# Optimization experiments

Measured on AMD Instinct MI355X. Metric: run time of the kernel, lower is better.

## Reference

```python
import jax, jax.numpy as jnp
import numpy as np

ROW = COL = 8   # unfold tile size
KS = 5          # gaussian raster kernel size
C1 = 6          # high-freq feature split

def conv2d(x, w, b=None, pad=0):
    y = jax.lax.conv_general_dilated(x, w, (1, 1), [(pad, pad), (pad, pad)],
                                     dimension_numbers=('NCHW', 'OIHW', 'NCHW'))
    if b is not None:
        y = y + b[None, :, None, None]
    return y

def unfold_tiles(x, r, c):
    # non-overlapping Unfold(kernel=(r,c), stride=(r,c)) -> [B*L, C, r, c]
    B, C, H, W = x.shape
    x = x.reshape(B, C, H // r, r, W // c, c).transpose(0, 2, 4, 1, 3, 5)
    return x.reshape(B * (H // r) * (W // c), C, r, c)

def fold_tiles(t, B, C, H, W, r, c):
    t = t.reshape(B, H // r, W // c, C, r, c).transpose(0, 3, 1, 4, 2, 5)
    return t.reshape(B, C, H, W)

def setup_inputs() -> dict:
    key = jax.random.key(0)
    ks = jax.random.split(key, 16)
    B, NF, H, W, P = 32, 48, 128, 128, 81
    inp = {
        'ms': jax.random.normal(ks[0], (B, 4, 32, 32), jnp.float32),
        'feat': jax.random.normal(ks[1], (B, NF, H, W), jnp.float32),
        'V': jax.random.normal(ks[2], (B, NF, H, W), jnp.float32),
        'logits_raw': jax.random.normal(ks[3], (B, P, H, W), jnp.float32),
        'sigma_x': jax.random.uniform(ks[4], (P,), jnp.float32, 0.2, 3.0),
        'sigma_y': jax.random.uniform(ks[5], (P,), jnp.float32, 0.2, 3.0),
        'opacity': jax.random.uniform(ks[6], (P,), jnp.float32, 0.1, 1.0),
        'rho': jax.random.uniform(ks[7], (P,), jnp.float32, -0.9, 0.9),
        'w_v2': jax.random.normal(ks[8], (42, 42, 1, 1), jnp.float32) * 0.05,
        'w_fine': jax.random.normal(ks[9], (4, NF, 3, 3), jnp.float32) * 0.05,
        'b_fine': jax.random.normal(ks[10], (4,), jnp.float32) * 0.05,
        'w_res': jax.random.normal(ks[11], (4, NF, 1, 1), jnp.float32) * 0.05,
        'b_res': jax.random.normal(ks[12], (4,), jnp.float32) * 0.05,
    }
    return inp

def reference(ms, feat, V, logits_raw, sigma_x, sigma_y, opacity, rho,
              w_v2, w_fine, b_fine, w_res, b_res):
    B, nf, H, W = feat.shape
    # soft class assignment (gumbel_softmax tau=1, zero-noise deterministic surrogate)
    logits = jax.nn.softmax(logits_raw, axis=1)
    feat1, lr_feat = feat[:, :C1], feat[:, C1:]
    V1, V2 = V[:, :C1], V[:, C1:]
    # H,W are already multiples of ROW/COL -> bicubic-to-same-size is identity
    uf = unfold_tiles(feat1, ROW, COL)        # [B*L, c1, 8, 8]
    ul = unfold_tiles(logits, ROW, COL)       # [B*L, P, 8, 8]
    uv1 = unfold_tiles(V1, ROW, COL)          # [B*L, c1, 8, 8]
    # weighted gaussian params per in-tile position, averaged over all tiles
    pm = ul.reshape(ul.shape[0], ul.shape[1], -1).mean(axis=0)   # [P, 64]
    wsx = sigma_x @ pm; wsy = sigma_y @ pm                       # [64]
    wop = opacity @ pm; wr = rho @ pm                            # [64]
    # 2x2 covariance per point, analytic inverse
    a = wsx ** 2; bcv = wr * wsx * wsy; d = wsy ** 2
    det = a * d - bcv ** 2
    i00 = d / det; i01 = -bcv / det; i11 = a / det
    ax = jnp.linspace(-5.0, 5.0, KS)
    xx = ax[:, None]; yy = ax[None, :]
    z = -0.5 * (i00[:, None, None] * xx ** 2 + 2.0 * i01[:, None, None] * xx * yy
                + i11[:, None, None] * yy ** 2)
    kern = jnp.exp(z) / (2.0 * jnp.pi * jnp.sqrt(det))[:, None, None]   # [64, KS, KS]
    kern = kern / kern.max(axis=(-2, -1), keepdims=True)
    kern = kern * wop[:, None, None]
    # splat: place each point's kernel centered at its grid position in the 8x8 tile
    pad = KS // 2
    ii = jnp.arange(ROW * COL) // COL
    jj = jnp.arange(ROW * COL) % COL
    canvas = jnp.zeros((ROW + 2 * pad, COL + 2 * pad), kern.dtype)
    place = jax.vmap(lambda k, i, j: jax.lax.dynamic_update_slice(canvas, k, (i, j)))
    K = place(kern, ii, jj)[:, pad:pad + ROW, pad:pad + COL]             # [64, 8, 8]
    colors = uf.reshape(uf.shape[0], C1, ROW * COL)                      # [N, c1, 64]
    rendered = jnp.einsum('ncp,phw->nchw', colors, K) * uv1              # modulate by V1
    hr = fold_tiles(rendered, B, C1, H, W, ROW, COL)                     # [B, c1, H, W]
    # squeeze-style channel attention on low branch, modulated by V2
    gap = lr_feat.mean(axis=(2, 3), keepdims=True)
    attn = jax.nn.sigmoid(conv2d(gap, w_v2))
    lr_mod = lr_feat * attn * V2
    out_feat = jnp.concatenate([hr, lr_mod], axis=1)                     # [B, n_feats, H, W]
    up_ms = jax.image.resize(ms, (B, ms.shape[1], H, W), method='bilinear')
    out = conv2d(out_feat, w_fine, b_fine, pad=1) + conv2d(feat, w_res, b_res) + up_ms
    return out
```

## Files before the change

### kernel.cpp

```cpp
#include <hip/hip_runtime.h>

#define NBATCH 32
#define NFEAT 48
#define C1c 6
#define LRC 42
#define HH 128
#define WW 128
#define HWSZ 16384
#define NP 81
#define NQ 64

#define OFF_PM   0
#define OFF_GAP  5184
#define OFF_K    6528
#define OFF_ATTN 10624
#define OFF_WB   11968
#define OFF_HR   14272

__global__ __launch_bounds__(256) void k_sm1(const float* __restrict__ logits,
                                             float* __restrict__ invbuf) {
    int idx = blockIdx.x * 256 + threadIdx.x;
    int b   = idx >> 14;
    int pos = idx & 16383;
    const float* base = logits + (((size_t)b * NP) << 14) + pos;
    float s = 0.f;
    for (int p = 0; p < NP; ++p)
        s += __expf(base[(size_t)p << 14]);
    invbuf[idx] = 1.f / s;
}

__global__ __launch_bounds__(256) void k_base(const float* __restrict__ feat,
                                              const float* __restrict__ ms,
                                              const float* __restrict__ w_res,
                                              const float* __restrict__ b_fine,
                                              const float* __restrict__ b_res,
                                              float* __restrict__ gap,
                                              float* __restrict__ out) {
    int gid = blockIdx.x;
    int tid = threadIdx.x;
    int b = gid >> 4, strip = gid & 15;
    int row = (strip << 3) + (tid >> 5);
    int x0  = (tid & 31) << 2;
    int poff = (row << 7) + x0;
    int lane = tid & 63;
    const float* fb = feat + (((size_t)b * NFEAT) << 14);
    float a[4][4];
#pragma unroll
    for (int j = 0; j < 4; ++j)
#pragma unroll
        for (int o = 0; o < 4; ++o) a[j][o] = 0.f;
    for (int c = 0; c < NFEAT; ++c) {
        float4 f = *(const float4*)&fb[((size_t)c << 14) + poff];
        float wr0 = w_res[c], wr1 = w_res[NFEAT + c];
        float wr2 = w_res[2 * NFEAT + c], wr3 = w_res[3 * NFEAT + c];
        a[0][0] += wr0 * f.x; a[0][1] += wr1 * f.x; a[0][2] += wr2 * f.x; a[0][3] += wr3 * f.x;
        a[1][0] += wr0 * f.y; a[1][1] += wr1 * f.y; a[1][2] += wr2 * f.y; a[1][3] += wr3 * f.y;
        a[2][0] += wr0 * f.z; a[2][1] += wr1 * f.z; a[2][2] += wr2 * f.z; a[2][3] += wr3 * f.z;
        a[3][0] += wr0 * f.w; a[3][1] += wr1 * f.w; a[3][2] += wr2 * f.w; a[3][3] += wr3 * f.w;
        if (c >= C1c) {
            float s = (f.x + f.y) + (f.z + f.w);
            s += __shfl_xor(s, 1);  s += __shfl_xor(s, 2);  s += __shfl_xor(s, 4);
            s += __shfl_xor(s, 8);  s += __shfl_xor(s, 16); s += __shfl_xor(s, 32);
            if (lane == 0) atomicAdd(&gap[b * LRC + (c - C1c)], s);
        }
    }
    float syf = (row + 0.5f) * 0.25f - 0.5f;
    int y0i = (int)floorf(syf); float fy = syf - (float)y0i;
    int y0c = min(31, max(0, y0i)), y1c = min(31, max(0, y0i + 1));
    float fxv[4]; int x0v[4], x1v[4];
#pragma unroll
    for (int j = 0; j < 4; ++j) {
        float sxf = (x0 + j + 0.5f) * 0.25f - 0.5f;
        int x0i = (int)floorf(sxf);
        fxv[j] = sxf - (float)x0i;
        x0v[j] = min(31, max(0, x0i));
        x1v[j] = min(31, max(0, x0i + 1));
    }
#pragma unroll
    for (int o = 0; o < 4; ++o) {
        const float* mb = ms + ((size_t)(b * 4 + o) << 10);
        float addc = b_fine[o] + b_res[o];
        float res[4];
#pragma unroll
        for (int j = 0; j < 4; ++j) {
            float m00 = mb[(y0c << 5) + x0v[j]], m01 = mb[(y0c << 5) + x1v[j]];
            float m10 = mb[(y1c << 5) + x0v[j]], m11 = mb[(y1c << 5) + x1v[j]];
            float up = (m00 * (1.f - fxv[j]) + m01 * fxv[j]) * (1.f - fy)
                     + (m10 * (1.f - fxv[j]) + m11 * fxv[j]) * fy;
            res[j] = a[j][o] + addc + up;
        }
        *(float4*)&out[(((size_t)(b * 4 + o)) << 14) + poff] =
            make_float4(res[0], res[1], res[2], res[3]);
    }
}

__global__ __launch_bounds__(256) void k_sm2(const float* __restrict__ logits,
                                             const float* __restrict__ invbuf,
                                             float* __restrict__ pm_sum) {
    int bid = blockIdx.x;
    int b = bid / NP, p = bid - b * NP;
    const float* base = logits + ((size_t)(b * NP + p) << 14);
    const float* ib   = invbuf + ((size_t)b << 14);
    int tid = threadIdx.x;
    int r0 = tid >> 5, xt = tid & 31;
    float a0 = 0.f, a1 = 0.f, a2 = 0.f, a3 = 0.f;
    int off = (r0 << 7) + (xt << 2);
#pragma unroll 4
    for (int k = 0; k < 16; ++k) {
        int o2 = off + k * 1024;
        float4 l4 = *(const float4*)&base[o2];
        float4 i4 = *(const float4*)&ib[o2];
        a0 += __expf(l4.x) * i4.x;
        a1 += __expf(l4.y) * i4.y;
        a2 += __expf(l4.z) * i4.z;
        a3 += __expf(l4.w) * i4.w;
    }
#pragma unroll
    for (int m = 2; m <= 16; m <<= 1) {
        a0 += __shfl_xor(a0, m); a1 += __shfl_xor(a1, m);
        a2 += __shfl_xor(a2, m); a3 += __shfl_xor(a3, m);
    }
    if (xt < 2) {
        int qb = p * NQ + (r0 << 3) + ((xt & 1) << 2);
        atomicAdd(&pm_sum[qb + 0], a0);
        atomicAdd(&pm_sum[qb + 1], a1);
        atomicAdd(&pm_sum[qb + 2], a2);
        atomicAdd(&pm_sum[qb + 3], a3);
    }
}

__global__ __launch_bounds__(256) void k_small(const float* __restrict__ pm_sum,
                                               const float* __restrict__ gap_sum,
                                               const float* __restrict__ sigx,
                                               const float* __restrict__ sigy,
                                               const float* __restrict__ opac,
                                               const float* __restrict__ rho,
                                               const float* __restrict__ w_v2,
                                               const float* __restrict__ w_fine,
                                               const float* __restrict__ w_res,
                                               float* __restrict__ Kmat,
                                               float* __restrict__ attn,
                                               float* __restrict__ wbuf) {
    int tid = threadIdx.x;
    if (tid < 64) {
        int q = tid;
        float wsx = 0.f, wsy = 0.f, wop = 0.f, wr = 0.f;
        for (int p = 0; p < NP; ++p) {
            float pv = pm_sum[p * NQ + q] * (1.f / 8192.f);
            wsx += sigx[p] * pv;
            wsy += sigy[p] * pv;
            wop += opac[p] * pv;
            wr  += rho[p]  * pv;
        }
        float a = wsx * wsx, d = wsy * wsy, bc = wr * wsx * wsy;
        float det = a * d - bc * bc;
        float i00 = d / det, i01 = -bc / det, i11 = a / det;
        int iq = q >> 3, jq = q & 7;
        for (int h = 0; h < 8; ++h)
            for (int w = 0; w < 8; ++w) {
                int ki = h - iq + 2, kj = w - jq + 2;
                float val = 0.f;
                if (ki >= 0 && ki < 5 && kj >= 0 && kj < 5) {
                    float xx = -5.f + 2.5f * ki, yy = -5.f + 2.5f * kj;
                    val = wop * __expf(-0.5f * (i00 * xx * xx + 2.f * i01 * xx * yy + i11 * yy * yy));
                }
                Kmat[(q << 6) + (h << 3) + w] = val;
            }
    }
    for (int i = tid; i < NBATCH * LRC; i += 256) {
        int b = i / LRC, co = i % LRC;
        float s = 0.f;
        for (int ci = 0; ci < LRC; ++ci) s += w_v2[co * LRC + ci] * gap_sum[b * LRC + ci];
        s *= (1.f / 16384.f);
        attn[i] = 1.f / (1.f + __expf(-s));
    }
    for (int i = tid; i < NFEAT * 48; i += 256) {
        int c = i / 48, j = i - c * 48;
        float v = 0.f;
        if (j < 36) v = w_fine[(j / 9) * (NFEAT * 9) + c * 9 + (j % 9)];
        else if (j < 40) v = w_res[(j - 36) * NFEAT + c];
        wbuf[i] = v;
    }
}

__global__ __launch_bounds__(256) void k_hr(const float* __restrict__ feat,
                                            const float* __restrict__ V,
                                            const float* __restrict__ Kmat,
                                            float* __restrict__ hrbuf) {
    __shared__ __align__(16) float lK[4096];
    __shared__ __align__(16) float lF[2 * 16 * 128];
    int bid = blockIdx.x;
    int b   = bid / 24;
    int r   = bid - b * 24;
    int strip = r / 3;
    int ch  = (r - strip * 3) * 2;
    int y0  = strip << 4;
    int tid = threadIdx.x;
    {
        const float4* ks = (const float4*)Kmat;
        float4* kd = (float4*)lK;
        for (int i = tid; i < 1024; i += 256) kd[i] = ks[i];
        float4* fd = (float4*)lF;
        const float* fb = feat + (((size_t)b * NFEAT + ch) << 14) + (y0 << 7);
        for (int i = tid; i < 1024; i += 256) {
            int c = i >> 9, rem = i & 511;
            fd[i] = *(const float4*)&fb[((size_t)c << 14) + (rem << 2)];
        }
    }
    __syncthreads();
    int tile = tid >> 3, hrow = tid & 7;
    int tr = tile >> 4, tx = tile & 15;
    float acc[2][8];
#pragma unroll
    for (int c = 0; c < 2; ++c)
#pragma unroll
        for (int j = 0; j < 8; ++j) acc[c][j] = 0.f;
    int fbase = (tr << 3) * 128 + (tx << 3);
    for (int q = 0; q < 64; ++q) {
        int iq = q >> 3, jq = q & 7;
        const float4 k0 = *(const float4*)&lK[(q << 6) + (hrow << 3)];
        const float4 k1 = *(const float4*)&lK[(q << 6) + (hrow << 3) + 4];
#pragma unroll
        for (int c = 0; c < 2; ++c) {
            float col = lF[(c << 11) + fbase + (iq << 7) + jq];
            acc[c][0] += col * k0.x; acc[c][1] += col * k0.y;
            acc[c][2] += col * k0.z; acc[c][3] += col * k0.w;
            acc[c][4] += col * k1.x; acc[c][5] += col * k1.y;
            acc[c][6] += col * k1.z; acc[c][7] += col * k1.w;
        }
    }
    int y = y0 + (tr << 3) + hrow;
#pragma unroll
    for (int c = 0; c < 2; ++c) {
        const float4* vp = (const float4*)(V + (((size_t)b * NFEAT + ch + c) << 14) + ((size_t)y << 7) + (tx << 3));
        float4 v0 = vp[0], v1 = vp[1];
        float4 r0, r1;
        r0.x = acc[c][0] * v0.x; r0.y = acc[c][1] * v0.y; r0.z = acc[c][2] * v0.z; r0.w = acc[c][3] * v0.w;
        r1.x = acc[c][4] * v1.x; r1.y = acc[c][5] * v1.y; r1.z = acc[c][6] * v1.z; r1.w = acc[c][7] * v1.w;
        float4* op = (float4*)(hrbuf + (((size_t)b * C1c + ch + c) << 14) + ((size_t)y << 7) + (tx << 3));
        op[0] = r0; op[1] = r1;
    }
}

#define CHN 6
__global__ __launch_bounds__(512, 4) void k_conv(const float* __restrict__ feat,
                                                 const float* __restrict__ V,
                                                 const float* __restrict__ wbuf,
                                                 const float* __restrict__ hrbuf,
                                                 const float* __restrict__ attn,
                                                 float* __restrict__ out) {
    __shared__ float s_in[2][CHN][18 * 40];
    int bid0 = blockIdx.x;
    int rid  = (bid0 & 7) * 128 + (bid0 >> 3);
    int b    = rid >> 5;
    int t32  = rid & 31;
    int ty0  = (t32 >> 2) << 4;
    int tx0  = (t32 & 3) << 5;
    int tid  = threadIdx.x;
    int grpu = __builtin_amdgcn_readfirstlane(tid >> 8);
    int ct   = tid & 255;
    int rp   = ct >> 5;
    int j    = ct & 31;
    int gx   = tx0 + j;
    int gy0  = ty0 + 2 * rp;
    int cbase = (2 * rp) * 40 + 3 + j;

    int srow = tid >> 5, scol = tid & 31;
    int sg = ((ty0 + srow) << 7) + tx0 + scol;
    int sl = (srow + 1) * 40 + 4 + scol;

    bool hhas = tid < 100;
    int rr, cc;
    if (tid < 34)      { rr = 0;        cc = tid; }
    else if (tid < 68) { rr = 17;       cc = tid - 34; }
    else if (tid < 84) { rr = tid - 67; cc = 0; }
    else               { rr = tid - 83; cc = 33; }
    int hsy = ty0 - 1 + rr, hsx = tx0 - 1 + cc;
    float hfm = (hsy >= 0 && hsy < HH && hsx >= 0 && hsx < WW) ? 1.f : 0.f;
    int hoff = (min(HH - 1, max(0, hsy)) << 7) + min(WW - 1, max(0, hsx));
    int hlds = rr * 40 + 3 + cc;

    const float* atb = attn + b * LRC;
    float a0[4] = {0.f, 0.f, 0.f, 0.f};
    float a1[4] = {0.f, 0.f, 0.f, 0.f};
    float rA[CHN], rB[CHN], rHA[CHN], rHB[CHN], amv[CHN];

#pragma unroll
    for (int k = 0; k < CHN; ++k) {
        const float* hs = hrbuf + (((size_t)(b * C1c + k)) << 14);
        rA[k]  = hs[sg];
        rHA[k] = hhas ? hs[hoff] : 0.f;
    }
#pragma unroll
    for (int k = 0; k < CHN; ++k) {
        s_in[0][k][sl] = rA[k];
        if (hhas) s_in[0][k][hlds] = rHA[k] * hfm;
    }
    int cur = 0;
    for (int t = 0; t < 8; ++t) {
        __syncthreads();
        if (t < 7) {
            int c0 = CHN * (t + 1);
#pragma unroll
            for (int k = 0; k < CHN; ++k) {
                int c = c0 + k;
                const float* fs = feat + (((size_t)(b * NFEAT + c)) << 14);
                const float* vs = V    + (((size_t)(b * NFEAT + c)) << 14);
                rA[k] = fs[sg];
                rB[k] = vs[sg];
                amv[k] = atb[c - C1c];
                rHA[k] = hhas ? fs[hoff] : 0.f;
                rHB[k] = hhas ? vs[hoff] : 0.f;
            }
        }
        int c0c = CHN * t;
        for (int k = 0; k < 3; ++k) {
            int slot = 3 * grpu + k;
            int c = c0c + slot;
            const float* wc = wbuf + c * 48;
            const float* sp = &s_in[cur][slot][cbase];
            float t00 = sp[0],   t01 = sp[1],   t02 = sp[2];
            float t10 = sp[40],  t11 = sp[41],  t12 = sp[42];
            float t20 = sp[80],  t21 = sp[81],  t22 = sp[82];
            float t30 = sp[120], t31 = sp[121], t32 = sp[122];
#pragma unroll
            for (int o = 0; o < 4; ++o) {
                float w0 = wc[o * 9 + 0], w1 = wc[o * 9 + 1], w2 = wc[o * 9 + 2];
                float w3 = wc[o * 9 + 3], w4 = wc[o * 9 + 4], w5 = wc[o * 9 + 5];
                float w6 = wc[o * 9 + 6], w7 = wc[o * 9 + 7], w8 = wc[o * 9 + 8];
                a0[o] += w0 * t00 + w1 * t01 + w2 * t02
                       + w3 * t10 + w4 * t11 + w5 * t12
                       + w6 * t20 + w7 * t21 + w8 * t22;
                a1[o] += w0 * t10 + w1 * t11 + w2 * t12
                       + w3 * t20 + w4 * t21 + w5 * t22
                       + w6 * t30 + w7 * t31 + w8 * t32;
            }
        }
        if (t < 7) {
            int nxt = cur ^ 1;
#pragma unroll
            for (int k = 0; k < CHN; ++k) {
                s_in[nxt][k][sl] = rA[k] * rB[k] * amv[k];
                if (hhas) s_in[nxt][k][hlds] = rHA[k] * rHB[k] * (amv[k] * hfm);
            }
        }
        cur ^= 1;
    }
    __syncthreads();
    float* sm = &s_in[0][0][0];
    int p0 = (2 * rp) * 32 + j, p1 = p0 + 32;
    if (grpu == 1) {
#pragma unroll
        for (int o = 0; o < 4; ++o) { sm[o * 512 + p0] = a0[o]; sm[o * 512 + p1] = a1[o]; }
    }
    __syncthreads();
    if (grpu == 0) {
#pragma unroll
        for (int o = 0; o < 4; ++o) {
            size_t obase = ((size_t)(b * 4 + o)) << 14;
            float* op0 = out + obase + (gy0 << 7) + gx;
            float* op1 = out + obase + ((gy0 + 1) << 7) + gx;
            *op0 = *op0 + a0[o] + sm[o * 512 + p0];
            *op1 = *op1 + a1[o] + sm[o * 512 + p1];
        }
    }
}

extern "C" void kernel_launch(void* const* d_in, const int* in_sizes, int n_in,
                              void* d_out, int out_size, void* d_ws, size_t ws_size,
                              hipStream_t stream) {
    (void)in_sizes; (void)n_in; (void)out_size; (void)ws_size;
    const float* ms     = (const float*)d_in[0];
    const float* feat   = (const float*)d_in[1];
    const float* V      = (const float*)d_in[2];
    const float* logits = (const float*)d_in[3];
    const float* sigx   = (const float*)d_in[4];
    const float* sigy   = (const float*)d_in[5];
    const float* opac   = (const float*)d_in[6];
    const float* rho    = (const float*)d_in[7];
    const float* w_v2   = (const float*)d_in[8];
    const float* w_fine = (const float*)d_in[9];
    const float* b_fine = (const float*)d_in[10];
    const float* w_res  = (const float*)d_in[11];
    const float* b_res  = (const float*)d_in[12];
    float* ws  = (float*)d_ws;
    float* out = (float*)d_out;
    float* inv = ws + OFF_HR;

    hipMemsetAsync(ws + OFF_PM, 0, (size_t)(NP * NQ + NBATCH * LRC) * sizeof(float), stream);
    k_sm1<<<2048, 256, 0, stream>>>(logits, inv);
    k_base<<<512, 256, 0, stream>>>(feat, ms, w_res, b_fine, b_res, ws + OFF_GAP, out);
    k_sm2<<<NBATCH * NP, 256, 0, stream>>>(logits, inv, ws + OFF_PM);
    k_small<<<1, 256, 0, stream>>>(ws + OFF_PM, ws + OFF_GAP, sigx, sigy, opac, rho, w_v2,
                                   w_fine, w_res, ws + OFF_K, ws + OFF_ATTN, ws + OFF_WB);
    k_hr<<<768, 256, 0, stream>>>(feat, V, ws + OFF_K, ws + OFF_HR);
    k_conv<<<1024, 512, 0, stream>>>(feat, V, ws + OFF_WB, ws + OFF_HR, ws + OFF_ATTN, out);
}
```

Baseline: 216.5 us.

## Split softmax denominator into channel-chunked partial sums plus reduction kernel

The per-pixel softmax denominator pass now splits the 81 logit channels into 9 chunks per batch. Each block streams a whole channel plane with float4 loads and writes partial exp-sums to a new workspace region. A second small kernel sums the 9 partials and writes reciprocals. This aims to raise memory-level parallelism and load width over the old one-thread-per-pixel 81-deep strided loop, at the cost of an extra launch and a partial buffer round trip.

Result: slower. 276.2 us (+27.6%).

```diff
diff --git a/kernel.cpp b/kernel.cpp
--- a/kernel.cpp
+++ b/kernel.cpp
@@ -16,17 +16,44 @@
 #define OFF_ATTN 10624
 #define OFF_WB   11968
 #define OFF_HR   14272
+#define OFF_PART (OFF_HR + 4194304)
 
 __global__ __launch_bounds__(256) void k_sm1(const float* __restrict__ logits,
-                                             float* __restrict__ invbuf) {
+                                             float* __restrict__ part) {
+    int bid = blockIdx.x;
+    int b = bid / 9, chunk = bid - b * 9;
+    int p0 = chunk * 9;
+    int tid = threadIdx.x;
+    const float4* lg4 = (const float4*)logits;
+    float4 acc[16];
+#pragma unroll
+    for (int k = 0; k < 16; ++k) acc[k] = make_float4(0.f, 0.f, 0.f, 0.f);
+    for (int i = 0; i < 9; ++i) {
+        const float4* pl = lg4 + ((size_t)(b * NP + p0 + i) << 12);
+#pragma unroll
+        for (int k = 0; k < 16; ++k) {
+            float4 v = pl[(k << 8) + tid];
+            acc[k].x += __expf(v.x); acc[k].y += __expf(v.y);
+            acc[k].z += __expf(v.z); acc[k].w += __expf(v.w);
+        }
+    }
+    float4* pp = (float4*)part + ((size_t)bid << 12);
+#pragma unroll
+    for (int k = 0; k < 16; ++k) pp[(k << 8) + tid] = acc[k];
+}
+
+__global__ __launch_bounds__(256) void k_minv(const float* __restrict__ part,
+                                              float* __restrict__ invbuf) {
     int idx = blockIdx.x * 256 + threadIdx.x;
-    int b   = idx >> 14;
-    int pos = idx & 16383;
-    const float* base = logits + (((size_t)b * NP) << 14) + pos;
-    float s = 0.f;
-    for (int p = 0; p < NP; ++p)
-        s += __expf(base[(size_t)p << 14]);
-    invbuf[idx] = 1.f / s;
+    int b = idx >> 12, i = idx & 4095;
+    const float4* p4 = (const float4*)part;
+    float sx = 0.f, sy = 0.f, sz = 0.f, sw = 0.f;
+#pragma unroll
+    for (int c = 0; c < 9; ++c) {
+        float4 v = p4[((size_t)(b * 9 + c) << 12) + i];
+        sx += v.x; sy += v.y; sz += v.z; sw += v.w;
+    }
+    ((float4*)invbuf)[idx] = make_float4(1.f / sx, 1.f / sy, 1.f / sz, 1.f / sw);
 }
 
 __global__ __launch_bounds__(256) void k_base(const float* __restrict__ feat,
@@ -385,11 +412,13 @@
     const float* b_res  = (const float*)d_in[12];
     float* ws  = (float*)d_ws;
     float* out = (float*)d_out;
-    float* inv = ws + OFF_HR;
+    float* inv  = ws + OFF_HR;
+    float* part = ws + OFF_PART;
 
     hipMemsetAsync(ws + OFF_PM, 0, (size_t)(NP * NQ + NBATCH * LRC) * sizeof(float), stream);
-    k_sm1<<<2048, 256, 0, stream>>>(logits, inv);
+    k_sm1<<<288, 256, 0, stream>>>(logits, part);
     k_base<<<512, 256, 0, stream>>>(feat, ms, w_res, b_fine, b_res, ws + OFF_GAP, out);
+    k_minv<<<512, 256, 0, stream>>>(part, inv);
     k_sm2<<<NBATCH * NP, 256, 0, stream>>>(logits, inv, ws + OFF_PM);
     k_small<<<1, 256, 0, stream>>>(ws + OFF_PM, ws + OFF_GAP, sigx, sigy, opac, rho, w_v2,
                                    w_fine, w_res, ws + OFF_K, ws + OFF_ATTN, ws + OFF_WB);
```

## Split softmax denominator over class chunks and fuse with base conv kernel

Applied to the files above, without the earlier changes.

The softmax sum-of-exp pass is split into three chunks of 27 classes, each computed by separate blocks with hand-written double-buffered dwordx4 loads. These blocks are merged into one launch with the residual conv/upsample blocks so both independent passes run concurrently. A small kernel then sums the three partial results and takes the reciprocal. This adds a partial buffer round trip and an extra launch, in exchange for more parallelism, wider loads and overlap of the two memory-bound passes.

Result: faster. 210.3 us (-2.8%).

```diff
diff --git a/kernel.cpp b/kernel.cpp
--- a/kernel.cpp
+++ b/kernel.cpp
@@ -16,82 +16,121 @@
 #define OFF_ATTN 10624
 #define OFF_WB   11968
 #define OFF_HR   14272
-
-__global__ __launch_bounds__(256) void k_sm1(const float* __restrict__ logits,
-                                             float* __restrict__ invbuf) {
+#define OFF_PART (OFF_HR + 4194304)
+
+typedef float f4 __attribute__((ext_vector_type(4)));
+
+#define GL(dst, ptr) asm volatile("global_load_dwordx4 %0, %1, off" : "=v"(dst) : "v"(ptr))
+#define WAITV2()     asm volatile("s_waitcnt vmcnt(2)" ::: "memory")
+#define WAITV0()     asm volatile("s_waitcnt vmcnt(0)" ::: "memory")
+#define SBAR()       __builtin_amdgcn_sched_barrier(0)
+
+__global__ __launch_bounds__(256) void k_phase1(const float* __restrict__ logits,
+                                                const float* __restrict__ feat,
+                                                const float* __restrict__ ms,
+                                                const float* __restrict__ w_res,
+                                                const float* __restrict__ b_fine,
+                                                const float* __restrict__ b_res,
+                                                float* __restrict__ part,
+                                                float* __restrict__ gap,
+                                                float* __restrict__ out) {
+    int bid = blockIdx.x;
+    int tid = threadIdx.x;
+    if (bid < 768) {
+        int s = bid >> 8;
+        int r = bid & 255;
+        int b = r >> 3, w = r & 7;
+        const float* base = logits + (((size_t)(b * NP + s * 27)) << 14) + (w << 11) + (tid << 3);
+        f4 A0 = {0.f, 0.f, 0.f, 0.f}, A1 = {0.f, 0.f, 0.f, 0.f};
+        f4 c0, c1, n0, n1;
+        GL(c0, base); GL(c1, base + 4);
+        for (int p = 0; p < 26; p += 2) {
+            const float* p1 = base + ((size_t)(p + 1) << 14);
+            GL(n0, p1); GL(n1, p1 + 4);
+            WAITV2(); SBAR();
+            A0.x += __expf(c0.x); A0.y += __expf(c0.y); A0.z += __expf(c0.z); A0.w += __expf(c0.w);
+            A1.x += __expf(c1.x); A1.y += __expf(c1.y); A1.z += __expf(c1.z); A1.w += __expf(c1.w);
+            const float* p2 = base + ((size_t)(p + 2) << 14);
+            GL(c0, p2); GL(c1, p2 + 4);
+            WAITV2(); SBAR();
+            A0.x += __expf(n0.x); A0.y += __expf(n0.y); A0.z += __expf(n0.z); A0.w += __expf(n0.w);
+            A1.x += __expf(n1.x); A1.y += __expf(n1.y); A1.z += __expf(n1.z); A1.w += __expf(n1.w);
+        }
+        WAITV0(); SBAR();
+        A0.x += __expf(c0.x); A0.y += __expf(c0.y); A0.z += __expf(c0.z); A0.w += __expf(c0.w);
+        A1.x += __expf(c1.x); A1.y += __expf(c1.y); A1.z += __expf(c1.z); A1.w += __expf(c1.w);
+        float* pp = part + (size_t)s * 524288 + ((size_t)b << 14) + (w << 11) + (tid << 3);
+        *(f4*)pp = A0;
+        *(f4*)(pp + 4) = A1;
+    } else {
+        int gid = bid - 768;
+        int b = gid >> 4, strip = gid & 15;
+        int row = (strip << 3) + (tid >> 5);
+        int x0  = (tid & 31) << 2;
+        int poff = (row << 7) + x0;
+        int lane = tid & 63;
+        const float* fb = feat + (((size_t)b * NFEAT) << 14);
+        float a[4][4];
+#pragma unroll
+        for (int j = 0; j < 4; ++j)
+#pragma unroll
+            for (int o = 0; o < 4; ++o) a[j][o] = 0.f;
+        for (int c = 0; c < NFEAT; ++c) {
+            float4 f = *(const float4*)&fb[((size_t)c << 14) + poff];
+            float wr0 = w_res[c], wr1 = w_res[NFEAT + c];
+            float wr2 = w_res[2 * NFEAT + c], wr3 = w_res[3 * NFEAT + c];
+            a[0][0] += wr0 * f.x; a[0][1] += wr1 * f.x; a[0][2] += wr2 * f.x; a[0][3] += wr3 * f.x;
+            a[1][0] += wr0 * f.y; a[1][1] += wr1 * f.y; a[1][2] += wr2 * f.y; a[1][3] += wr3 * f.y;
+            a[2][0] += wr0 * f.z; a[2][1] += wr1 * f.z; a[2][2] += wr2 * f.z; a[2][3] += wr3 * f.z;
+            a[3][0] += wr0 * f.w; a[3][1] += wr1 * f.w; a[3][2] += wr2 * f.w; a[3][3] += wr3 * f.w;
+            if (c >= C1c) {
+                float s = (f.x + f.y) + (f.z + f.w);
+                s += __shfl_xor(s, 1);  s += __shfl_xor(s, 2);  s += __shfl_xor(s, 4);
+                s += __shfl_xor(s, 8);  s += __shfl_xor(s, 16); s += __shfl_xor(s, 32);
+                if (lane == 0) atomicAdd(&gap[b * LRC + (c - C1c)], s);
+            }
+        }
+        float syf = (row + 0.5f) * 0.25f - 0.5f;
+        int y0i = (int)floorf(syf); float fy = syf - (float)y0i;
+        int y0c = min(31, max(0, y0i)), y1c = min(31, max(0, y0i + 1));
+        float fxv[4]; int x0v[4], x1v[4];
+#pragma unroll
+        for (int j = 0; j < 4; ++j) {
+            float sxf = (x0 + j + 0.5f) * 0.25f - 0.5f;
+            int x0i = (int)floorf(sxf);
+            fxv[j] = sxf - (float)x0i;
+            x0v[j] = min(31, max(0, x0i));
+            x1v[j] = min(31, max(0, x0i + 1));
+        }
+#pragma unroll
+        for (int o = 0; o < 4; ++o) {
+            const float* mb = ms + ((size_t)(b * 4 + o) << 10);
+            float addc = b_fine[o] + b_res[o];
+            float res[4];
+#pragma unroll
+            for (int j = 0; j < 4; ++j) {
+                float m00 = mb[(y0c << 5) + x0v[j]], m01 = mb[(y0c << 5) + x1v[j]];
+                float m10 = mb[(y1c << 5) + x0v[j]], m11 = mb[(y1c << 5) + x1v[j]];
+                float up = (m00 * (1.f - fxv[j]) + m01 * fxv[j]) * (1.f - fy)
+                         + (m10 * (1.f - fxv[j]) + m11 * fxv[j]) * fy;
+                res[j] = a[j][o] + addc + up;
+            }
+            *(float4*)&out[(((size_t)(b * 4 + o)) << 14) + poff] =
+                make_float4(res[0], res[1], res[2], res[3]);
+        }
+    }
+}
+
+__global__ __launch_bounds__(256) void k_minv(const float* __restrict__ part,
+                                              float* __restrict__ invbuf) {
     int idx = blockIdx.x * 256 + threadIdx.x;
-    int b   = idx >> 14;
-    int pos = idx & 16383;
-    const float* base = logits + (((size_t)b * NP) << 14) + pos;
-    float s = 0.f;
-    for (int p = 0; p < NP; ++p)
-        s += __expf(base[(size_t)p << 14]);
-    invbuf[idx] = 1.f / s;
-}
-
-__global__ __launch_bounds__(256) void k_base(const float* __restrict__ feat,
-                                              const float* __restrict__ ms,
-                                              const float* __restrict__ w_res,
-                                              const float* __restrict__ b_fine,
-                                              const float* __restrict__ b_res,
-                                              float* __restrict__ gap,
-                                              float* __restrict__ out) {
-    int gid = blockIdx.x;
-    int tid = threadIdx.x;
-    int b = gid >> 4, strip = gid & 15;
-    int row = (strip << 3) + (tid >> 5);
-    int x0  = (tid & 31) << 2;
-    int poff = (row << 7) + x0;
-    int lane = tid & 63;
-    const float* fb = feat + (((size_t)b * NFEAT) << 14);
-    float a[4][4];
-#pragma unroll
-    for (int j = 0; j < 4; ++j)
-#pragma unroll
-        for (int o = 0; o < 4; ++o) a[j][o] = 0.f;
-    for (int c = 0; c < NFEAT; ++c) {
-        float4 f = *(const float4*)&fb[((size_t)c << 14) + poff];
-        float wr0 = w_res[c], wr1 = w_res[NFEAT + c];
-        float wr2 = w_res[2 * NFEAT + c], wr3 = w_res[3 * NFEAT + c];
-        a[0][0] += wr0 * f.x; a[0][1] += wr1 * f.x; a[0][2] += wr2 * f.x; a[0][3] += wr3 * f.x;
-        a[1][0] += wr0 * f.y; a[1][1] += wr1 * f.y; a[1][2] += wr2 * f.y; a[1][3] += wr3 * f.y;
-        a[2][0] += wr0 * f.z; a[2][1] += wr1 * f.z; a[2][2] += wr2 * f.z; a[2][3] += wr3 * f.z;
-        a[3][0] += wr0 * f.w; a[3][1] += wr1 * f.w; a[3][2] += wr2 * f.w; a[3][3] += wr3 * f.w;
-        if (c >= C1c) {
-            float s = (f.x + f.y) + (f.z + f.w);
-            s += __shfl_xor(s, 1);  s += __shfl_xor(s, 2);  s += __shfl_xor(s, 4);
-            s += __shfl_xor(s, 8);  s += __shfl_xor(s, 16); s += __shfl_xor(s, 32);
-            if (lane == 0) atomicAdd(&gap[b * LRC + (c - C1c)], s);
-        }
-    }
-    float syf = (row + 0.5f) * 0.25f - 0.5f;
-    int y0i = (int)floorf(syf); float fy = syf - (float)y0i;
-    int y0c = min(31, max(0, y0i)), y1c = min(31, max(0, y0i + 1));
-    float fxv[4]; int x0v[4], x1v[4];
-#pragma unroll
-    for (int j = 0; j < 4; ++j) {
-        float sxf = (x0 + j + 0.5f) * 0.25f - 0.5f;
-        int x0i = (int)floorf(sxf);
-        fxv[j] = sxf - (float)x0i;
-        x0v[j] = min(31, max(0, x0i));
-        x1v[j] = min(31, max(0, x0i + 1));
-    }
-#pragma unroll
-    for (int o = 0; o < 4; ++o) {
-        const float* mb = ms + ((size_t)(b * 4 + o) << 10);
-        float addc = b_fine[o] + b_res[o];
-        float res[4];
-#pragma unroll
-        for (int j = 0; j < 4; ++j) {
-            float m00 = mb[(y0c << 5) + x0v[j]], m01 = mb[(y0c << 5) + x1v[j]];
-            float m10 = mb[(y1c << 5) + x0v[j]], m11 = mb[(y1c << 5) + x1v[j]];
-            float up = (m00 * (1.f - fxv[j]) + m01 * fxv[j]) * (1.f - fy)
-                     + (m10 * (1.f - fxv[j]) + m11 * fxv[j]) * fy;
-            res[j] = a[j][o] + addc + up;
-        }
-        *(float4*)&out[(((size_t)(b * 4 + o)) << 14) + poff] =
-            make_float4(res[0], res[1], res[2], res[3]);
-    }
+    const f4* p4 = (const f4*)part;
+    f4 a = p4[idx];
+    f4 b = p4[idx + 131072];
+    f4 c = p4[idx + 262144];
+    f4 s = a + b + c;
+    f4 r = {1.f / s.x, 1.f / s.y, 1.f / s.z, 1.f / s.w};
+    ((f4*)invbuf)[idx] = r;
 }
 
 __global__ __launch_bounds__(256) void k_sm2(const float* __restrict__ logits,
@@ -385,11 +424,13 @@
     const float* b_res  = (const float*)d_in[12];
     float* ws  = (float*)d_ws;
     float* out = (float*)d_out;
-    float* inv = ws + OFF_HR;
+    float* inv  = ws + OFF_HR;
+    float* part = ws + OFF_PART;
 
     hipMemsetAsync(ws + OFF_PM, 0, (size_t)(NP * NQ + NBATCH * LRC) * sizeof(float), stream);
-    k_sm1<<<2048, 256, 0, stream>>>(logits, inv);
-    k_base<<<512, 256, 0, stream>>>(feat, ms, w_res, b_fine, b_res, ws + OFF_GAP, out);
+    k_phase1<<<768 + 512, 256, 0, stream>>>(logits, feat, ms, w_res, b_fine, b_res,
+                                            part, ws + OFF_GAP, out);
+    k_minv<<<512, 256, 0, stream>>>(part, inv);
     k_sm2<<<NBATCH * NP, 256, 0, stream>>>(logits, inv, ws + OFF_PM);
     k_small<<<1, 256, 0, stream>>>(ws + OFF_PM, ws + OFF_GAP, sigx, sigy, opac, rho, w_v2,
                                    w_fine, w_res, ws + OFF_K, ws + OFF_ATTN, ws + OFF_WB);
```

## Fuse softmax passes into single-read kernel merged with base conv blocks

Applied to the files above, without the earlier changes.

Replaces the two-pass softmax (one kernel for the inverse sums, a second that re-reads logits) with a single pass. Each thread keeps all 81 exponentials in registers, normalises them, and accumulates per-tile sums that are reduced with shuffles and atomics. This kernel is merged with the residual-conv/upsample blocks into one launch, with separate block ranges for each job. It removes a full second read of the logits plus the intermediate inverse buffer. In exchange it uses heavy register arrays (81 accumulators plus 81 exponentials), which can hurt occupancy or spill under launch_bounds(256,2).

Result: faster. 188.7 us, median of 2 (-12.8%).

```diff
diff --git a/kernel.cpp b/kernel.cpp
--- a/kernel.cpp
+++ b/kernel.cpp
@@ -17,115 +17,102 @@
 #define OFF_WB   11968
 #define OFF_HR   14272
 
-__global__ __launch_bounds__(256) void k_sm1(const float* __restrict__ logits,
-                                             float* __restrict__ invbuf) {
-    int idx = blockIdx.x * 256 + threadIdx.x;
-    int b   = idx >> 14;
-    int pos = idx & 16383;
-    const float* base = logits + (((size_t)b * NP) << 14) + pos;
-    float s = 0.f;
-    for (int p = 0; p < NP; ++p)
-        s += __expf(base[(size_t)p << 14]);
-    invbuf[idx] = 1.f / s;
-}
-
-__global__ __launch_bounds__(256) void k_base(const float* __restrict__ feat,
-                                              const float* __restrict__ ms,
-                                              const float* __restrict__ w_res,
-                                              const float* __restrict__ b_fine,
-                                              const float* __restrict__ b_res,
-                                              float* __restrict__ gap,
-                                              float* __restrict__ out) {
-    int gid = blockIdx.x;
+__global__ __launch_bounds__(256, 2) void k_phase1(const float* __restrict__ logits,
+                                                   const float* __restrict__ feat,
+                                                   const float* __restrict__ ms,
+                                                   const float* __restrict__ w_res,
+                                                   const float* __restrict__ b_fine,
+                                                   const float* __restrict__ b_res,
+                                                   float* __restrict__ pm_sum,
+                                                   float* __restrict__ gap,
+                                                   float* __restrict__ out) {
+    int bid = blockIdx.x;
     int tid = threadIdx.x;
-    int b = gid >> 4, strip = gid & 15;
-    int row = (strip << 3) + (tid >> 5);
-    int x0  = (tid & 31) << 2;
-    int poff = (row << 7) + x0;
-    int lane = tid & 63;
-    const float* fb = feat + (((size_t)b * NFEAT) << 14);
-    float a[4][4];
-#pragma unroll
-    for (int j = 0; j < 4; ++j)
-#pragma unroll
-        for (int o = 0; o < 4; ++o) a[j][o] = 0.f;
-    for (int c = 0; c < NFEAT; ++c) {
-        float4 f = *(const float4*)&fb[((size_t)c << 14) + poff];
-        float wr0 = w_res[c], wr1 = w_res[NFEAT + c];
-        float wr2 = w_res[2 * NFEAT + c], wr3 = w_res[3 * NFEAT + c];
-        a[0][0] += wr0 * f.x; a[0][1] += wr1 * f.x; a[0][2] += wr2 * f.x; a[0][3] += wr3 * f.x;
-        a[1][0] += wr0 * f.y; a[1][1] += wr1 * f.y; a[1][2] += wr2 * f.y; a[1][3] += wr3 * f.y;
-        a[2][0] += wr0 * f.z; a[2][1] += wr1 * f.z; a[2][2] += wr2 * f.z; a[2][3] += wr3 * f.z;
-        a[3][0] += wr0 * f.w; a[3][1] += wr1 * f.w; a[3][2] += wr2 * f.w; a[3][3] += wr3 * f.w;
-        if (c >= C1c) {
-            float s = (f.x + f.y) + (f.z + f.w);
-            s += __shfl_xor(s, 1);  s += __shfl_xor(s, 2);  s += __shfl_xor(s, 4);
-            s += __shfl_xor(s, 8);  s += __shfl_xor(s, 16); s += __shfl_xor(s, 32);
-            if (lane == 0) atomicAdd(&gap[b * LRC + (c - C1c)], s);
-        }
-    }
-    float syf = (row + 0.5f) * 0.25f - 0.5f;
-    int y0i = (int)floorf(syf); float fy = syf - (float)y0i;
-    int y0c = min(31, max(0, y0i)), y1c = min(31, max(0, y0i + 1));
-    float fxv[4]; int x0v[4], x1v[4];
-#pragma unroll
-    for (int j = 0; j < 4; ++j) {
-        float sxf = (x0 + j + 0.5f) * 0.25f - 0.5f;
-        int x0i = (int)floorf(sxf);
-        fxv[j] = sxf - (float)x0i;
-        x0v[j] = min(31, max(0, x0i));
-        x1v[j] = min(31, max(0, x0i + 1));
-    }
-#pragma unroll
-    for (int o = 0; o < 4; ++o) {
-        const float* mb = ms + ((size_t)(b * 4 + o) << 10);
-        float addc = b_fine[o] + b_res[o];
-        float res[4];
+    if (bid < 512) {
+        int b   = bid >> 4;
+        int ygp = (bid >> 2) & 3;
+        int qq  = bid & 3;
+        int x   = tid & 127;
+        int yg  = ygp * 2 + (tid >> 7);
+        float acc[NP];
+#pragma unroll
+        for (int p = 0; p < NP; ++p) acc[p] = 0.f;
+        for (int k = 0; k < 4; ++k) {
+            int y = yg + 8 * (qq * 4 + k);
+            const float* base = logits + (size_t)b * NP * HWSZ + (y << 7) + x;
+            float ev[NP];
+            float s = 0.f;
+#pragma unroll
+            for (int p = 0; p < NP; ++p) { ev[p] = __expf(base[(size_t)p * HWSZ]); s += ev[p]; }
+            float inv = 1.f / s;
+#pragma unroll
+            for (int p = 0; p < NP; ++p) acc[p] += ev[p] * inv;
+        }
+        int lane = tid & 63;
+#pragma unroll
+        for (int p = 0; p < NP; ++p) {
+            float e = acc[p];
+            e += __shfl_xor(e, 8);
+            e += __shfl_xor(e, 16);
+            e += __shfl_xor(e, 32);
+            if (lane < 8) atomicAdd(&pm_sum[p * NQ + (yg << 3) + lane], e);
+        }
+    } else {
+        int gid = bid - 512;
+        int b = gid >> 4, strip = gid & 15;
+        int row = (strip << 3) + (tid >> 5);
+        int x0  = (tid & 31) << 2;
+        int poff = (row << 7) + x0;
+        int lane = tid & 63;
+        const float* fb = feat + (((size_t)b * NFEAT) << 14);
+        float a[4][4];
+#pragma unroll
+        for (int j = 0; j < 4; ++j)
+#pragma unroll
+            for (int o = 0; o < 4; ++o) a[j][o] = 0.f;
+        for (int c = 0; c < NFEAT; ++c) {
+            float4 f = *(const float4*)&fb[((size_t)c << 14) + poff];
+            float wr0 = w_res[c], wr1 = w_res[NFEAT + c];
+            float wr2 = w_res[2 * NFEAT + c], wr3 = w_res[3 * NFEAT + c];
+            a[0][0] += wr0 * f.x; a[0][1] += wr1 * f.x; a[0][2] += wr2 * f.x; a[0][3] += wr3 * f.x;
+            a[1][0] += wr0 * f.y; a[1][1] += wr1 * f.y; a[1][2] += wr2 * f.y; a[1][3] += wr3 * f.y;
+            a[2][0] += wr0 * f.z; a[2][1] += wr1 * f.z; a[2][2] += wr2 * f.z; a[2][3] += wr3 * f.z;
+            a[3][0] += wr0 * f.w; a[3][1] += wr1 * f.w; a[3][2] += wr2 * f.w; a[3][3] += wr3 * f.w;
+            if (c >= C1c) {
+                float s = (f.x + f.y) + (f.z + f.w);
+                s += __shfl_xor(s, 1);  s += __shfl_xor(s, 2);  s += __shfl_xor(s, 4);
+                s += __shfl_xor(s, 8);  s += __shfl_xor(s, 16); s += __shfl_xor(s, 32);
+                if (lane == 0) atomicAdd(&gap[b * LRC + (c - C1c)], s);
+            }
+        }
+        float syf = (row + 0.5f) * 0.25f - 0.5f;
+        int y0i = (int)floorf(syf); float fy = syf - (float)y0i;
+        int y0c = min(31, max(0, y0i)), y1c = min(31, max(0, y0i + 1));
+        float fxv[4]; int x0v[4], x1v[4];
 #pragma unroll
         for (int j = 0; j < 4; ++j) {
-            float m00 = mb[(y0c << 5) + x0v[j]], m01 = mb[(y0c << 5) + x1v[j]];
-            float m10 = mb[(y1c << 5) + x0v[j]], m11 = mb[(y1c << 5) + x1v[j]];
-            float up = (m00 * (1.f - fxv[j]) + m01 * fxv[j]) * (1.f - fy)
-                     + (m10 * (1.f - fxv[j]) + m11 * fxv[j]) * fy;
-            res[j] = a[j][o] + addc + up;
-        }
-        *(float4*)&out[(((size_t)(b * 4 + o)) << 14) + poff] =
-            make_float4(res[0], res[1], res[2], res[3]);
-    }
-}
-
-__global__ __launch_bounds__(256) void k_sm2(const float* __restrict__ logits,
-                                             const float* __restrict__ invbuf,
-                                             float* __restrict__ pm_sum) {
-    int bid = blockIdx.x;
-    int b = bid / NP, p = bid - b * NP;
-    const float* base = logits + ((size_t)(b * NP + p) << 14);
-    const float* ib   = invbuf + ((size_t)b << 14);
-    int tid = threadIdx.x;
-    int r0 = tid >> 5, xt = tid & 31;
-    float a0 = 0.f, a1 = 0.f, a2 = 0.f, a3 = 0.f;
-    int off = (r0 << 7) + (xt << 2);
-#pragma unroll 4
-    for (int k = 0; k < 16; ++k) {
-        int o2 = off + k * 1024;
-        float4 l4 = *(const float4*)&base[o2];
-        float4 i4 = *(const float4*)&ib[o2];
-        a0 += __expf(l4.x) * i4.x;
-        a1 += __expf(l4.y) * i4.y;
-        a2 += __expf(l4.z) * i4.z;
-        a3 += __expf(l4.w) * i4.w;
-    }
-#pragma unroll
-    for (int m = 2; m <= 16; m <<= 1) {
-        a0 += __shfl_xor(a0, m); a1 += __shfl_xor(a1, m);
-        a2 += __shfl_xor(a2, m); a3 += __shfl_xor(a3, m);
-    }
-    if (xt < 2) {
-        int qb = p * NQ + (r0 << 3) + ((xt & 1) << 2);
-        atomicAdd(&pm_sum[qb + 0], a0);
-        atomicAdd(&pm_sum[qb + 1], a1);
-        atomicAdd(&pm_sum[qb + 2], a2);
-        atomicAdd(&pm_sum[qb + 3], a3);
+            float sxf = (x0 + j + 0.5f) * 0.25f - 0.5f;
+            int x0i = (int)floorf(sxf);
+            fxv[j] = sxf - (float)x0i;
+            x0v[j] = min(31, max(0, x0i));
+            x1v[j] = min(31, max(0, x0i + 1));
+        }
+#pragma unroll
+        for (int o = 0; o < 4; ++o) {
+            const float* mb = ms + ((size_t)(b * 4 + o) << 10);
+            float addc = b_fine[o] + b_res[o];
+            float res[4];
+#pragma unroll
+            for (int j = 0; j < 4; ++j) {
+                float m00 = mb[(y0c << 5) + x0v[j]], m01 = mb[(y0c << 5) + x1v[j]];
+                float m10 = mb[(y1c << 5) + x0v[j]], m11 = mb[(y1c << 5) + x1v[j]];
+                float up = (m00 * (1.f - fxv[j]) + m01 * fxv[j]) * (1.f - fy)
+                         + (m10 * (1.f - fxv[j]) + m11 * fxv[j]) * fy;
+                res[j] = a[j][o] + addc + up;
+            }
+            *(float4*)&out[(((size_t)(b * 4 + o)) << 14) + poff] =
+                make_float4(res[0], res[1], res[2], res[3]);
+        }
     }
 }
 
@@ -385,12 +372,10 @@
     const float* b_res  = (const float*)d_in[12];
     float* ws  = (float*)d_ws;
     float* out = (float*)d_out;
-    float* inv = ws + OFF_HR;
 
     hipMemsetAsync(ws + OFF_PM, 0, (size_t)(NP * NQ + NBATCH * LRC) * sizeof(float), stream);
-    k_sm1<<<2048, 256, 0, stream>>>(logits, inv);
-    k_base<<<512, 256, 0, stream>>>(feat, ms, w_res, b_fine, b_res, ws + OFF_GAP, out);
-    k_sm2<<<NBATCH * NP, 256, 0, stream>>>(logits, inv, ws + OFF_PM);
+    k_phase1<<<512 + 512, 256, 0, stream>>>(logits, feat, ms, w_res, b_fine, b_res,
+                                            ws + OFF_PM, ws + OFF_GAP, out);
     k_small<<<1, 256, 0, stream>>>(ws + OFF_PM, ws + OFF_GAP, sigx, sigy, opac, rho, w_v2,
                                    w_fine, w_res, ws + OFF_K, ws + OFF_ATTN, ws + OFF_WB);
     k_hr<<<768, 256, 0, stream>>>(feat, V, ws + OFF_K, ws + OFF_HR);
```
